# Kernel optimization log

Measured on AMD Instinct MI355X. Metric: run time of the kernel, lower is better.

## Reference

```python
import jax, jax.numpy as jnp
import numpy as np

N = 512          # hidden size n
B = 256          # batch
T = 512          # timesteps
INPUT_SIZE = 2
RANK = 2
ALPHA = 0.2
SIGMA_IN = 0.2
SIGMA_REC = 0.15


def setup_inputs() -> dict:
    key = jax.random.key(0)
    k1, k2, k3, k4, k5, k6 = jax.random.split(key, 6)
    u = jax.random.normal(k1, (B, T, INPUT_SIZE), dtype=jnp.float32)
    # standard normal; scaled by sqrt(2/alpha*sigma_in^2) inside reference
    input_noise = jax.random.normal(k2, (B, T, INPUT_SIZE), dtype=jnp.float32)
    # in the repo this is sigma_rec * randn projected on PCs; plain scaled randn here
    recurrent_noise = SIGMA_REC * jax.random.normal(k3, (B, T, N), dtype=jnp.float32)
    # low-rank recurrent weight: W_rec = A @ B, entries ~ U(-0.1, 0.1)
    A = 0.1 * (2.0 * jax.random.uniform(k4, (N, RANK), dtype=jnp.float32) - 1.0)
    Bm = 0.1 * (2.0 * jax.random.uniform(k5, (RANK, N), dtype=jnp.float32) - 1.0)
    W_rec = A @ Bm
    b_rec = jnp.zeros((N,), dtype=jnp.float32)  # normal_(std=0) -> zeros
    # nn.Linear default init: U(-1/sqrt(in), 1/sqrt(in))
    bound = 1.0 / np.sqrt(INPUT_SIZE)
    W_in = jax.random.uniform(k6, (N, INPUT_SIZE), dtype=jnp.float32,
                              minval=-bound, maxval=bound)
    return {"u": u, "input_noise": input_noise, "recurrent_noise": recurrent_noise,
            "W_in": W_in, "W_rec": W_rec, "b_rec": b_rec}


def reference(u, input_noise, recurrent_noise, W_in, W_rec, b_rec):
    alpha = ALPHA
    in_scale = np.sqrt(2.0 / ALPHA * SIGMA_IN ** 2).astype(np.float32)
    # inputs = input_layer(u + input_noise)  -> [B, T, N]
    inputs = jnp.einsum('bti,ni->btn', u + in_scale * input_noise, W_in)
    # scan over first T-1 timesteps, time-major
    xs = (jnp.swapaxes(inputs, 0, 1)[:-1],          # [T-1, B, N]
          jnp.swapaxes(recurrent_noise, 0, 1)[:-1])  # [T-1, B, N]
    s0 = jnp.zeros((u.shape[0], W_rec.shape[0]), dtype=u.dtype)

    def step(s, x):
        inp_t, noise_t = x
        s_new = (1.0 - alpha) * s + alpha * (
            jax.nn.relu(s) @ W_rec.T + b_rec + inp_t + noise_t)
        return s_new, s_new

    _, ys = jax.lax.scan(step, s0, xs)              # [T-1, B, N]
    states = jnp.concatenate([s0[None], ys], axis=0)  # [T, B, N]
    return jnp.swapaxes(states, 0, 1)               # [B, T, N]
```

## Files before the change

### kernel.cpp

```cpp
#include <hip/hip_runtime.h>
#include <math.h>

#define NH 512
#define BATCH 256
#define TT 512
#define NSTEPS 511
#define ALPHA 0.2f
#define OMA 0.8f
#define ISCALE 0.6324555320336759f
#define PD 12
#define WPB 4

typedef float vf2 __attribute__((ext_vector_type(2)));
typedef float vf4 __attribute__((ext_vector_type(4)));


__device__ __forceinline__ float wave_reduce_sum(float v) {
#pragma unroll
    for (int m = 32; m >= 1; m >>= 1) v += __shfl_xor(v, m, 64);
    return v;
}

__device__ __forceinline__ unsigned long long enc_key(float v, int i) {
    return (((unsigned long long)__float_as_uint(v)) << 32) | (unsigned int)i;
}

__device__ __forceinline__ unsigned long long wave_max_key(unsigned long long k) {
#pragma unroll
    for (int m = 32; m >= 1; m >>= 1) {
        unsigned long long o = __shfl_xor(k, m, 64);
        k = (o > k) ? o : k;
    }
    return k;
}

__device__ __forceinline__ int scan_argmax_rn(const float* __restrict__ rn, int tid) {
    const float4* rn4 = (const float4*)rn;
    unsigned long long key = 0;
#pragma unroll
    for (int r = 0; r < 2; ++r) {
        float4 v = rn4[tid + 64 * r];
        int base = 4 * (tid + 64 * r);
        unsigned long long k0 = enc_key(v.x, base);
        unsigned long long k1 = enc_key(v.y, base + 1);
        unsigned long long k2 = enc_key(v.z, base + 2);
        unsigned long long k3 = enc_key(v.w, base + 3);
        k0 = k0 > k1 ? k0 : k1;
        k2 = k2 > k3 ? k2 : k3;
        k0 = k0 > k2 ? k0 : k2;
        key = key > k0 ? key : k0;
    }
    return (int)(wave_max_key(key) & 0xffffffffULL);
}

__device__ __forceinline__ float dpp_sum63(float v) {
    v += __int_as_float(__builtin_amdgcn_update_dpp(0, __float_as_int(v), 0x111, 0xf, 0xf, true));
    v += __int_as_float(__builtin_amdgcn_update_dpp(0, __float_as_int(v), 0x112, 0xf, 0xf, true));
    v += __int_as_float(__builtin_amdgcn_update_dpp(0, __float_as_int(v), 0x114, 0xf, 0xf, true));
    v += __int_as_float(__builtin_amdgcn_update_dpp(0, __float_as_int(v), 0x118, 0xf, 0xf, true));
    v += __int_as_float(__builtin_amdgcn_update_dpp(0, __float_as_int(v), 0x142, 0xa, 0xf, true));
    v += __int_as_float(__builtin_amdgcn_update_dpp(0, __float_as_int(v), 0x143, 0xc, 0xf, true));
    return v;
}


__global__ void k_rownorm(const float* __restrict__ W, float* __restrict__ rn) {
    const int i = blockIdx.x, tid = threadIdx.x;
    const float4* row = (const float4*)(W + (size_t)i * NH);
    float acc = 0.f;
#pragma unroll
    for (int r = 0; r < 2; ++r) {
        float4 v = row[tid + 64 * r];
        acc = fmaf(v.x, v.x, fmaf(v.y, v.y, fmaf(v.z, v.z, fmaf(v.w, v.w, acc))));
    }
    acc = wave_reduce_sum(acc);
    if (tid == 0) rn[i] = acc;
}

__global__ void k_rowdot(const float* __restrict__ W, const float* __restrict__ rn,
                         float* __restrict__ dv) {
    const int i = blockIdx.x, tid = threadIdx.x;
    const int i1 = scan_argmax_rn(rn, tid);
    const float4* rowi = (const float4*)(W + (size_t)i * NH);
    const float4* row1 = (const float4*)(W + (size_t)i1 * NH);
    float acc = 0.f;
#pragma unroll
    for (int r = 0; r < 2; ++r) {
        float4 a = rowi[tid + 64 * r];
        float4 b = row1[tid + 64 * r];
        acc = fmaf(a.x, b.x, fmaf(a.y, b.y, fmaf(a.z, b.z, fmaf(a.w, b.w, acc))));
    }
    acc = wave_reduce_sum(acc);
    if (tid == 0) dv[i] = acc;
}

__global__ void k_computeP(const float* __restrict__ W, const float* __restrict__ rn,
                           const float* __restrict__ dv, float* __restrict__ P,
                           int* __restrict__ idx) {
    const int n = blockIdx.x, tid = threadIdx.x;
    const int i1 = scan_argmax_rn(rn, tid);
    const float rn1 = rn[i1];
    const float inv1 = 1.f / rn1;

    const float4* rn4 = (const float4*)rn;
    const float4* dv4 = (const float4*)dv;
    unsigned long long key = 0;
#pragma unroll
    for (int r = 0; r < 2; ++r) {
        float4 a = rn4[tid + 64 * r];
        float4 d = dv4[tid + 64 * r];
        int base = 4 * (tid + 64 * r);
        float r0 = fmaxf(a.x - d.x * d.x * inv1, 0.f);
        float r1 = fmaxf(a.y - d.y * d.y * inv1, 0.f);
        float r2 = fmaxf(a.z - d.z * d.z * inv1, 0.f);
        float r3 = fmaxf(a.w - d.w * d.w * inv1, 0.f);
        unsigned long long k0 = (base + 0 != i1) ? enc_key(r0, base + 0) : 0ULL;
        unsigned long long k1 = (base + 1 != i1) ? enc_key(r1, base + 1) : 0ULL;
        unsigned long long k2 = (base + 2 != i1) ? enc_key(r2, base + 2) : 0ULL;
        unsigned long long k3 = (base + 3 != i1) ? enc_key(r3, base + 3) : 0ULL;
        k0 = k0 > k1 ? k0 : k1;
        k2 = k2 > k3 ? k2 : k3;
        k0 = k0 > k2 ? k0 : k2;
        key = key > k0 ? key : k0;
    }
    const int i2 = (int)(wave_max_key(key) & 0xffffffffULL);

    const float4* rown = (const float4*)(W + (size_t)n * NH);
    const float4* row1 = (const float4*)(W + (size_t)i1 * NH);
    const float4* row2 = (const float4*)(W + (size_t)i2 * NH);
    float t0 = 0.f, t1 = 0.f;
#pragma unroll
    for (int r = 0; r < 2; ++r) {
        float4 a = rown[tid + 64 * r];
        float4 b = row1[tid + 64 * r];
        float4 c = row2[tid + 64 * r];
        t0 = fmaf(a.x, b.x, fmaf(a.y, b.y, fmaf(a.z, b.z, fmaf(a.w, b.w, t0))));
        t1 = fmaf(a.x, c.x, fmaf(a.y, c.y, fmaf(a.z, c.z, fmaf(a.w, c.w, t1))));
    }
    t0 = wave_reduce_sum(t0);
    t1 = wave_reduce_sum(t1);
    if (tid == 0) {
        float g11 = rn1, g22 = rn[i2], g12 = dv[i2];
        float det = fmaf(g11, g22, -g12 * g12);
        float inv = 1.f / det;
        P[2 * n]     = ALPHA * ((g22 * t0 - g12 * t1) * inv);
        P[2 * n + 1] = ALPHA * ((g11 * t1 - g12 * t0) * inv);
        if (n == 0) { idx[0] = i1; idx[1] = i2; }
    }
}

__launch_bounds__(256, 1)
__global__ void k_main(const float* __restrict__ u, const float* __restrict__ inoise,
                       const float* __restrict__ rnoise, const float* __restrict__ W_in,
                       const float* __restrict__ W, const float* __restrict__ b_rec,
                       const int* __restrict__ idx, const float* __restrict__ P,
                       float* __restrict__ out) {
    __shared__ __align__(16) float2 lds_x[TT];
    __shared__ __align__(16) float2 lds_p[2][WPB];
    const int b = blockIdx.x;
    const int tid = threadIdx.x;
    const int wid = tid >> 6;
    const int lane = tid & 63;
    const int i1 = idx[0];
    const int i2 = idx[1];

    {
        const float4* u4 = (const float4*)(u + (size_t)b * TT * 2);
        const float4* n4 = (const float4*)(inoise + (size_t)b * TT * 2);
        float4 a = u4[tid];
        float4 c = n4[tid];
        float4 x;
        x.x = fmaf(ISCALE, c.x, a.x);
        x.y = fmaf(ISCALE, c.y, a.y);
        x.z = fmaf(ISCALE, c.z, a.z);
        x.w = fmaf(ISCALE, c.w, a.w);
        ((float4*)lds_x)[tid] = x;
    }
    __syncthreads();

    const int n0 = (wid << 7) + (lane << 1);
    const float q0x = W[(size_t)i1 * NH + n0],     q0y = W[(size_t)i1 * NH + n0 + 1];
    const float q1x = W[(size_t)i2 * NH + n0],     q1y = W[(size_t)i2 * NH + n0 + 1];
    const float A0x = P[2 * n0],                   A1x = P[2 * n0 + 1];
    const float A0y = P[2 * n0 + 2],               A1y = P[2 * n0 + 3];
    const float w0x = ALPHA * W_in[2 * n0],        w1x = ALPHA * W_in[2 * n0 + 1];
    const float w0y = ALPHA * W_in[2 * n0 + 2],    w1y = ALPHA * W_in[2 * n0 + 3];
    const float cbx = ALPHA * b_rec[n0],           cby = ALPHA * b_rec[n0 + 1];
    float sx = 0.f, sy = 0.f;

    const float* nzb = rnoise + (size_t)b * TT * NH + n0;
    float* ob = out + (size_t)b * TT * NH + n0;

    vf2 z = {0.f, 0.f};
    __builtin_nontemporal_store(z, (vf2*)ob);

    vf2 buf[PD];
#pragma unroll
    for (int k = 0; k < PD; ++k) buf[k] = *(const vf2*)(nzb + (size_t)k * NH);

#define STEP(t_, k_, REFILL_, XX_, XY_)                                              \
    {                                                                                \
        const int t = (t_);                                                          \
        vf2 nz = buf[k_];                                                            \
        if (REFILL_) {                                                               \
            int tp = t + PD; if (tp > NSTEPS) tp = NSTEPS;     \
            buf[k_] = *(const vf2*)(nzb + (size_t)tp * NH);                          \
        }                                                                            \
        const float xx = (XX_);                                                      \
        const float xy = (XY_);                                                      \
        float rsx = fmaxf(sx, 0.f), rsy = fmaxf(sy, 0.f);                            \
        float pa = fmaf(rsy, q0y, rsx * q0x);                                        \
        float pb = fmaf(rsy, q1y, rsx * q1x);                                        \
        pa = dpp_sum63(pa);                                                          \
        pb = dpp_sum63(pb);                                                          \
             \
        float bx = fmaf(ALPHA, nz.x, cbx);                                           \
        bx = fmaf(w0x, xx, bx);                                                      \
        bx = fmaf(w1x, xy, bx);                                                      \
        bx = fmaf(OMA, sx, bx);                                                      \
        float by = fmaf(ALPHA, nz.y, cby);                                           \
        by = fmaf(w0y, xx, by);                                                      \
        by = fmaf(w1y, xy, by);                                                      \
        by = fmaf(OMA, sy, by);                                                      \
        if (lane == 63) lds_p[(t) & 1][wid] = make_float2(pa, pb);                   \
        __syncthreads();                                                             \
        const float4* pp = (const float4*)lds_p[(t) & 1];                            \
        float4 r0 = pp[0];                                                           \
        float4 r1 = pp[1];                                                           \
        float p0 = (r0.x + r0.z) + (r1.x + r1.z);                                    \
        float p1 = (r0.y + r0.w) + (r1.y + r1.w);                                    \
        sx = fmaf(A1x, p1, fmaf(A0x, p0, bx));                                       \
        sy = fmaf(A1y, p1, fmaf(A0y, p0, by));                                       \
        vf2 o = {sx, sy};                                                            \
        __builtin_nontemporal_store(o, (vf2*)(ob + (size_t)(t + 1) * NH));           \
    }

    for (int tb = 0; tb < 504; tb += PD) {
        const float4* lxs = (const float4*)(lds_x + tb);
        float4 xb[6];
#pragma unroll
        for (int r = 0; r < 6; ++r) xb[r] = lxs[r];
#pragma unroll
        for (int k = 0; k < PD; ++k) {
            STEP(tb + k, k, true,
                 ((k & 1) ? xb[k >> 1].z : xb[k >> 1].x),
                 ((k & 1) ? xb[k >> 1].w : xb[k >> 1].y))
        }
    }
    {
        const float4* lxs = (const float4*)(lds_x + 504);
        float4 xb[4];
#pragma unroll
        for (int r = 0; r < 4; ++r) xb[r] = lxs[r];
#pragma unroll
        for (int k = 0; k < 7; ++k) {
            STEP(504 + k, k, false,
                 ((k & 1) ? xb[k >> 1].z : xb[k >> 1].x),
                 ((k & 1) ? xb[k >> 1].w : xb[k >> 1].y))
        }
    }

#undef STEP
}


extern "C" void kernel_launch(void* const* d_in, const int* in_sizes, int n_in,
                              void* d_out, int out_size, void* d_ws, size_t ws_size,
                              hipStream_t stream) {
    const float* u      = (const float*)d_in[0];
    const float* inoise = (const float*)d_in[1];
    const float* rnoise = (const float*)d_in[2];
    const float* W_in   = (const float*)d_in[3];
    const float* W      = (const float*)d_in[4];
    const float* b_rec  = (const float*)d_in[5];
    float* out = (float*)d_out;

    char* ws = (char*)d_ws;
    int* idx  = (int*)(ws + 0);
    float* rn = (float*)(ws + 64);
    float* dv = (float*)(ws + 2112);
    float* P  = (float*)(ws + 4160);

    hipLaunchKernelGGL(k_rownorm, dim3(NH), dim3(64), 0, stream, W, rn);
    hipLaunchKernelGGL(k_rowdot, dim3(NH), dim3(64), 0, stream, W, rn, dv);
    hipLaunchKernelGGL(k_computeP, dim3(NH), dim3(64), 0, stream, W, rn, dv, P, idx);
    hipLaunchKernelGGL(k_main, dim3(BATCH), dim3(256), 0, stream,
                       u, inoise, rnoise, W_in, W, b_rec, idx, P, out);
}
```

Before: 470.5 us.

## Fuse setup kernels into one block and use one element per thread

Merges the three projection-setup kernels into a single one-block kernel that keeps row norms and dot products in shared memory, which removes two launches and the workspace round-trips. The main recurrence kernel now uses 512 threads per block, each owning one hidden unit instead of two, and noise is read with nontemporal loads. This spreads per-step work over more waves, at the cost of a wider barrier and a larger cross-wave reduction each step, and the single-block setup serializes work over all rows.

```diff
diff --git a/kernel.cpp b/kernel.cpp
--- a/kernel.cpp
+++ b/kernel.cpp
@@ -9,10 +9,9 @@
 #define OMA 0.8f
 #define ISCALE 0.6324555320336759f
 #define PD 12
-#define WPB 4
+#define WPB 8
 
 typedef float vf2 __attribute__((ext_vector_type(2)));
-typedef float vf4 __attribute__((ext_vector_type(4)));
 
 
 __device__ __forceinline__ float wave_reduce_sum(float v) {
@@ -34,13 +33,13 @@
     return k;
 }
 
-__device__ __forceinline__ int scan_argmax_rn(const float* __restrict__ rn, int tid) {
+__device__ __forceinline__ int scan_argmax_rn(const float* __restrict__ rn, int lane) {
     const float4* rn4 = (const float4*)rn;
     unsigned long long key = 0;
 #pragma unroll
     for (int r = 0; r < 2; ++r) {
-        float4 v = rn4[tid + 64 * r];
-        int base = 4 * (tid + 64 * r);
+        float4 v = rn4[lane + 64 * r];
+        int base = 4 * (lane + 64 * r);
         unsigned long long k0 = enc_key(v.x, base);
         unsigned long long k1 = enc_key(v.y, base + 1);
         unsigned long long k2 = enc_key(v.z, base + 2);
@@ -64,52 +63,54 @@
 }
 
 
-__global__ void k_rownorm(const float* __restrict__ W, float* __restrict__ rn) {
-    const int i = blockIdx.x, tid = threadIdx.x;
-    const float4* row = (const float4*)(W + (size_t)i * NH);
-    float acc = 0.f;
+__global__ __launch_bounds__(256, 1)
+void k_setup(const float* __restrict__ W, float* __restrict__ P, int* __restrict__ idx) {
+    __shared__ __align__(16) float rn_s[NH];
+    __shared__ __align__(16) float dv_s[NH];
+    const int tid = threadIdx.x, wid = tid >> 6, lane = tid & 63;
+
+    for (int row = wid; row < NH; row += 4) {
+        const float4* r4 = (const float4*)(W + (size_t)row * NH);
+        float acc = 0.f;
+#pragma unroll
+        for (int r = 0; r < 2; ++r) {
+            float4 v = r4[lane + 64 * r];
+            acc = fmaf(v.x, v.x, fmaf(v.y, v.y, fmaf(v.z, v.z, fmaf(v.w, v.w, acc))));
+        }
+        acc = wave_reduce_sum(acc);
+        if (lane == 0) rn_s[row] = acc;
+    }
+    __syncthreads();
+
+    const int i1 = scan_argmax_rn(rn_s, lane);
+    const float rn1 = rn_s[i1];
+    const float inv1 = 1.f / rn1;
+
+    const float4* row1 = (const float4*)(W + (size_t)i1 * NH);
+    const float4 b0 = row1[lane], b1 = row1[lane + 64];
+
+    for (int row = wid; row < NH; row += 4) {
+        const float4* r4 = (const float4*)(W + (size_t)row * NH);
+        float acc = 0.f;
+        {
+            float4 a = r4[lane];
+            acc = fmaf(a.x, b0.x, fmaf(a.y, b0.y, fmaf(a.z, b0.z, fmaf(a.w, b0.w, acc))));
+            a = r4[lane + 64];
+            acc = fmaf(a.x, b1.x, fmaf(a.y, b1.y, fmaf(a.z, b1.z, fmaf(a.w, b1.w, acc))));
+        }
+        acc = wave_reduce_sum(acc);
+        if (lane == 0) dv_s[row] = acc;
+    }
+    __syncthreads();
+
+    const float4* rn4 = (const float4*)rn_s;
+    const float4* dv4 = (const float4*)dv_s;
+    unsigned long long key = 0;
 #pragma unroll
     for (int r = 0; r < 2; ++r) {
-        float4 v = row[tid + 64 * r];
-        acc = fmaf(v.x, v.x, fmaf(v.y, v.y, fmaf(v.z, v.z, fmaf(v.w, v.w, acc))));
-    }
-    acc = wave_reduce_sum(acc);
-    if (tid == 0) rn[i] = acc;
-}
-
-__global__ void k_rowdot(const float* __restrict__ W, const float* __restrict__ rn,
-                         float* __restrict__ dv) {
-    const int i = blockIdx.x, tid = threadIdx.x;
-    const int i1 = scan_argmax_rn(rn, tid);
-    const float4* rowi = (const float4*)(W + (size_t)i * NH);
-    const float4* row1 = (const float4*)(W + (size_t)i1 * NH);
-    float acc = 0.f;
-#pragma unroll
-    for (int r = 0; r < 2; ++r) {
-        float4 a = rowi[tid + 64 * r];
-        float4 b = row1[tid + 64 * r];
-        acc = fmaf(a.x, b.x, fmaf(a.y, b.y, fmaf(a.z, b.z, fmaf(a.w, b.w, acc))));
-    }
-    acc = wave_reduce_sum(acc);
-    if (tid == 0) dv[i] = acc;
-}
-
-__global__ void k_computeP(const float* __restrict__ W, const float* __restrict__ rn,
-                           const float* __restrict__ dv, float* __restrict__ P,
-                           int* __restrict__ idx) {
-    const int n = blockIdx.x, tid = threadIdx.x;
-    const int i1 = scan_argmax_rn(rn, tid);
-    const float rn1 = rn[i1];
-    const float inv1 = 1.f / rn1;
-
-    const float4* rn4 = (const float4*)rn;
-    const float4* dv4 = (const float4*)dv;
-    unsigned long long key = 0;
-#pragma unroll
-    for (int r = 0; r < 2; ++r) {
-        float4 a = rn4[tid + 64 * r];
-        float4 d = dv4[tid + 64 * r];
-        int base = 4 * (tid + 64 * r);
+        float4 a = rn4[lane + 64 * r];
+        float4 d = dv4[lane + 64 * r];
+        int base = 4 * (lane + 64 * r);
         float r0 = fmaxf(a.x - d.x * d.x * inv1, 0.f);
         float r1 = fmaxf(a.y - d.y * d.y * inv1, 0.f);
         float r2 = fmaxf(a.z - d.z * d.z * inv1, 0.f);
@@ -125,31 +126,33 @@
     }
     const int i2 = (int)(wave_max_key(key) & 0xffffffffULL);
 
-    const float4* rown = (const float4*)(W + (size_t)n * NH);
-    const float4* row1 = (const float4*)(W + (size_t)i1 * NH);
     const float4* row2 = (const float4*)(W + (size_t)i2 * NH);
-    float t0 = 0.f, t1 = 0.f;
-#pragma unroll
-    for (int r = 0; r < 2; ++r) {
-        float4 a = rown[tid + 64 * r];
-        float4 b = row1[tid + 64 * r];
-        float4 c = row2[tid + 64 * r];
-        t0 = fmaf(a.x, b.x, fmaf(a.y, b.y, fmaf(a.z, b.z, fmaf(a.w, b.w, t0))));
-        t1 = fmaf(a.x, c.x, fmaf(a.y, c.y, fmaf(a.z, c.z, fmaf(a.w, c.w, t1))));
-    }
-    t0 = wave_reduce_sum(t0);
-    t1 = wave_reduce_sum(t1);
-    if (tid == 0) {
-        float g11 = rn1, g22 = rn[i2], g12 = dv[i2];
-        float det = fmaf(g11, g22, -g12 * g12);
-        float inv = 1.f / det;
-        P[2 * n]     = ALPHA * ((g22 * t0 - g12 * t1) * inv);
-        P[2 * n + 1] = ALPHA * ((g11 * t1 - g12 * t0) * inv);
-        if (n == 0) { idx[0] = i1; idx[1] = i2; }
-    }
-}
-
-__launch_bounds__(256, 1)
+    const float4 c0 = row2[lane], c1 = row2[lane + 64];
+    const float g11 = rn1, g22 = rn_s[i2], g12 = dv_s[i2];
+    const float det = fmaf(g11, g22, -g12 * g12);
+    const float invd = 1.f / det;
+    for (int row = wid; row < NH; row += 4) {
+        const float4* r4 = (const float4*)(W + (size_t)row * NH);
+        float t0 = 0.f, t1 = 0.f;
+        {
+            float4 a = r4[lane];
+            t0 = fmaf(a.x, b0.x, fmaf(a.y, b0.y, fmaf(a.z, b0.z, fmaf(a.w, b0.w, t0))));
+            t1 = fmaf(a.x, c0.x, fmaf(a.y, c0.y, fmaf(a.z, c0.z, fmaf(a.w, c0.w, t1))));
+            a = r4[lane + 64];
+            t0 = fmaf(a.x, b1.x, fmaf(a.y, b1.y, fmaf(a.z, b1.z, fmaf(a.w, b1.w, t0))));
+            t1 = fmaf(a.x, c1.x, fmaf(a.y, c1.y, fmaf(a.z, c1.z, fmaf(a.w, c1.w, t1))));
+        }
+        t0 = wave_reduce_sum(t0);
+        t1 = wave_reduce_sum(t1);
+        if (lane == 0) {
+            P[2 * row]     = ALPHA * ((g22 * t0 - g12 * t1) * invd);
+            P[2 * row + 1] = ALPHA * ((g11 * t1 - g12 * t0) * invd);
+        }
+    }
+    if (tid == 0) { idx[0] = i1; idx[1] = i2; }
+}
+
+__launch_bounds__(512, 1)
 __global__ void k_main(const float* __restrict__ u, const float* __restrict__ inoise,
                        const float* __restrict__ rnoise, const float* __restrict__ W_in,
                        const float* __restrict__ W, const float* __restrict__ b_rec,
@@ -165,74 +168,67 @@
     const int i2 = idx[1];
 
     {
-        const float4* u4 = (const float4*)(u + (size_t)b * TT * 2);
-        const float4* n4 = (const float4*)(inoise + (size_t)b * TT * 2);
-        float4 a = u4[tid];
-        float4 c = n4[tid];
-        float4 x;
+        const float2* u2 = (const float2*)(u + (size_t)b * TT * 2);
+        const float2* n2 = (const float2*)(inoise + (size_t)b * TT * 2);
+        float2 a = u2[tid];
+        float2 c = n2[tid];
+        float2 x;
         x.x = fmaf(ISCALE, c.x, a.x);
         x.y = fmaf(ISCALE, c.y, a.y);
-        x.z = fmaf(ISCALE, c.z, a.z);
-        x.w = fmaf(ISCALE, c.w, a.w);
-        ((float4*)lds_x)[tid] = x;
+        lds_x[tid] = x;
     }
     __syncthreads();
 
-    const int n0 = (wid << 7) + (lane << 1);
-    const float q0x = W[(size_t)i1 * NH + n0],     q0y = W[(size_t)i1 * NH + n0 + 1];
-    const float q1x = W[(size_t)i2 * NH + n0],     q1y = W[(size_t)i2 * NH + n0 + 1];
-    const float A0x = P[2 * n0],                   A1x = P[2 * n0 + 1];
-    const float A0y = P[2 * n0 + 2],               A1y = P[2 * n0 + 3];
-    const float w0x = ALPHA * W_in[2 * n0],        w1x = ALPHA * W_in[2 * n0 + 1];
-    const float w0y = ALPHA * W_in[2 * n0 + 2],    w1y = ALPHA * W_in[2 * n0 + 3];
-    const float cbx = ALPHA * b_rec[n0],           cby = ALPHA * b_rec[n0 + 1];
-    float sx = 0.f, sy = 0.f;
+    const int n0 = (wid << 6) + lane;
+    const float q0 = W[(size_t)i1 * NH + n0];
+    const float q1 = W[(size_t)i2 * NH + n0];
+    const float A0 = P[2 * n0];
+    const float A1 = P[2 * n0 + 1];
+    const float w0 = ALPHA * W_in[2 * n0];
+    const float w1 = ALPHA * W_in[2 * n0 + 1];
+    const float cb = ALPHA * b_rec[n0];
+    float s = 0.f;
 
     const float* nzb = rnoise + (size_t)b * TT * NH + n0;
     float* ob = out + (size_t)b * TT * NH + n0;
 
-    vf2 z = {0.f, 0.f};
-    __builtin_nontemporal_store(z, (vf2*)ob);
-
-    vf2 buf[PD];
-#pragma unroll
-    for (int k = 0; k < PD; ++k) buf[k] = *(const vf2*)(nzb + (size_t)k * NH);
+    __builtin_nontemporal_store(0.f, ob);
+
+    float buf[PD];
+#pragma unroll
+    for (int k = 0; k < PD; ++k) buf[k] = __builtin_nontemporal_load(nzb + (size_t)k * NH);
 
 #define STEP(t_, k_, REFILL_, XX_, XY_)                                              \
     {                                                                                \
         const int t = (t_);                                                          \
-        vf2 nz = buf[k_];                                                            \
+        float nz = buf[k_];                                                          \
         if (REFILL_) {                                                               \
             int tp = t + PD; if (tp > NSTEPS) tp = NSTEPS;     \
-            buf[k_] = *(const vf2*)(nzb + (size_t)tp * NH);                          \
+            buf[k_] = __builtin_nontemporal_load(nzb + (size_t)tp * NH);             \
         }                                                                            \
         const float xx = (XX_);                                                      \
         const float xy = (XY_);                                                      \
-        float rsx = fmaxf(sx, 0.f), rsy = fmaxf(sy, 0.f);                            \
-        float pa = fmaf(rsy, q0y, rsx * q0x);                                        \
-        float pb = fmaf(rsy, q1y, rsx * q1x);                                        \
+        float rs = fmaxf(s, 0.f);                                                    \
+        float pa = rs * q0;                                                          \
+        float pb = rs * q1;                                                          \
         pa = dpp_sum63(pa);                                                          \
         pb = dpp_sum63(pb);                                                          \
              \
-        float bx = fmaf(ALPHA, nz.x, cbx);                                           \
-        bx = fmaf(w0x, xx, bx);                                                      \
-        bx = fmaf(w1x, xy, bx);                                                      \
-        bx = fmaf(OMA, sx, bx);                                                      \
-        float by = fmaf(ALPHA, nz.y, cby);                                           \
-        by = fmaf(w0y, xx, by);                                                      \
-        by = fmaf(w1y, xy, by);                                                      \
-        by = fmaf(OMA, sy, by);                                                      \
+        float base = fmaf(ALPHA, nz, cb);                                            \
+        base = fmaf(w0, xx, base);                                                   \
+        base = fmaf(w1, xy, base);                                                   \
+        base = fmaf(OMA, s, base);                                                   \
         if (lane == 63) lds_p[(t) & 1][wid] = make_float2(pa, pb);                   \
         __syncthreads();                                                             \
         const float4* pp = (const float4*)lds_p[(t) & 1];                            \
         float4 r0 = pp[0];                                                           \
         float4 r1 = pp[1];                                                           \
-        float p0 = (r0.x + r0.z) + (r1.x + r1.z);                                    \
-        float p1 = (r0.y + r0.w) + (r1.y + r1.w);                                    \
-        sx = fmaf(A1x, p1, fmaf(A0x, p0, bx));                                       \
-        sy = fmaf(A1y, p1, fmaf(A0y, p0, by));                                       \
-        vf2 o = {sx, sy};                                                            \
-        __builtin_nontemporal_store(o, (vf2*)(ob + (size_t)(t + 1) * NH));           \
+        float4 r2 = pp[2];                                                           \
+        float4 r3 = pp[3];                                                           \
+        float p0 = ((r0.x + r0.z) + (r1.x + r1.z)) + ((r2.x + r2.z) + (r3.x + r3.z));\
+        float p1 = ((r0.y + r0.w) + (r1.y + r1.w)) + ((r2.y + r2.w) + (r3.y + r3.w));\
+        s = fmaf(A1, p1, fmaf(A0, p0, base));                                        \
+        __builtin_nontemporal_store(s, ob + (size_t)(t + 1) * NH);                   \
     }
 
     for (int tb = 0; tb < 504; tb += PD) {
@@ -277,13 +273,9 @@
 
     char* ws = (char*)d_ws;
     int* idx  = (int*)(ws + 0);
-    float* rn = (float*)(ws + 64);
-    float* dv = (float*)(ws + 2112);
-    float* P  = (float*)(ws + 4160);
-
-    hipLaunchKernelGGL(k_rownorm, dim3(NH), dim3(64), 0, stream, W, rn);
-    hipLaunchKernelGGL(k_rowdot, dim3(NH), dim3(64), 0, stream, W, rn, dv);
-    hipLaunchKernelGGL(k_computeP, dim3(NH), dim3(64), 0, stream, W, rn, dv, P, idx);
-    hipLaunchKernelGGL(k_main, dim3(BATCH), dim3(256), 0, stream,
+    float* P  = (float*)(ws + 64);
+
+    hipLaunchKernelGGL(k_setup, dim3(1), dim3(256), 0, stream, W, P, idx);
+    hipLaunchKernelGGL(k_main, dim3(BATCH), dim3(512), 0, stream,
                        u, inoise, rnoise, W_in, W, b_rec, idx, P, out);
 }
```

Result: slower. 707.5 us (+50.4%).

## Use one hidden unit per thread with 512-thread blocks and lighter barrier

Applied to the files above, without the earlier changes.

Doubles the block to 512 threads so each thread owns a single hidden unit instead of two. This shortens the per-step dependent arithmetic and spreads the global loads and stores over more waves. The cross-wave partial sums now cover eight waves, and __syncthreads is replaced by an explicit lgkmcnt wait plus s_barrier. The cost is a barrier across eight waves instead of four, scalar rather than vector memory accesses, and a slightly longer LDS reduction at every step.

```diff
diff --git a/kernel.cpp b/kernel.cpp
--- a/kernel.cpp
+++ b/kernel.cpp
@@ -9,10 +9,9 @@
 #define OMA 0.8f
 #define ISCALE 0.6324555320336759f
 #define PD 12
-#define WPB 4
+#define WPB 8
 
 typedef float vf2 __attribute__((ext_vector_type(2)));
-typedef float vf4 __attribute__((ext_vector_type(4)));
 
 
 __device__ __forceinline__ float wave_reduce_sum(float v) {
@@ -149,7 +148,7 @@
     }
 }
 
-__launch_bounds__(256, 1)
+__launch_bounds__(512, 1)
 __global__ void k_main(const float* __restrict__ u, const float* __restrict__ inoise,
                        const float* __restrict__ rnoise, const float* __restrict__ W_in,
                        const float* __restrict__ W, const float* __restrict__ b_rec,
@@ -165,74 +164,70 @@
     const int i2 = idx[1];
 
     {
-        const float4* u4 = (const float4*)(u + (size_t)b * TT * 2);
-        const float4* n4 = (const float4*)(inoise + (size_t)b * TT * 2);
-        float4 a = u4[tid];
-        float4 c = n4[tid];
-        float4 x;
+        const float2* u2 = (const float2*)(u + (size_t)b * TT * 2);
+        const float2* n2 = (const float2*)(inoise + (size_t)b * TT * 2);
+        float2 a = u2[tid];
+        float2 c = n2[tid];
+        float2 x;
         x.x = fmaf(ISCALE, c.x, a.x);
         x.y = fmaf(ISCALE, c.y, a.y);
-        x.z = fmaf(ISCALE, c.z, a.z);
-        x.w = fmaf(ISCALE, c.w, a.w);
-        ((float4*)lds_x)[tid] = x;
+        lds_x[tid] = x;
     }
     __syncthreads();
 
-    const int n0 = (wid << 7) + (lane << 1);
-    const float q0x = W[(size_t)i1 * NH + n0],     q0y = W[(size_t)i1 * NH + n0 + 1];
-    const float q1x = W[(size_t)i2 * NH + n0],     q1y = W[(size_t)i2 * NH + n0 + 1];
-    const float A0x = P[2 * n0],                   A1x = P[2 * n0 + 1];
-    const float A0y = P[2 * n0 + 2],               A1y = P[2 * n0 + 3];
-    const float w0x = ALPHA * W_in[2 * n0],        w1x = ALPHA * W_in[2 * n0 + 1];
-    const float w0y = ALPHA * W_in[2 * n0 + 2],    w1y = ALPHA * W_in[2 * n0 + 3];
-    const float cbx = ALPHA * b_rec[n0],           cby = ALPHA * b_rec[n0 + 1];
-    float sx = 0.f, sy = 0.f;
+    const int n0 = (wid << 6) + lane;
+    const float q0 = W[(size_t)i1 * NH + n0];
+    const float q1 = W[(size_t)i2 * NH + n0];
+    const float A0 = P[2 * n0];
+    const float A1 = P[2 * n0 + 1];
+    const float w0 = ALPHA * W_in[2 * n0];
+    const float w1 = ALPHA * W_in[2 * n0 + 1];
+    const float cb = ALPHA * b_rec[n0];
+    float s = 0.f;
 
     const float* nzb = rnoise + (size_t)b * TT * NH + n0;
     float* ob = out + (size_t)b * TT * NH + n0;
 
-    vf2 z = {0.f, 0.f};
-    __builtin_nontemporal_store(z, (vf2*)ob);
-
-    vf2 buf[PD];
-#pragma unroll
-    for (int k = 0; k < PD; ++k) buf[k] = *(const vf2*)(nzb + (size_t)k * NH);
+    __builtin_nontemporal_store(0.f, ob);
+
+    float buf[PD];
+#pragma unroll
+    for (int k = 0; k < PD; ++k) buf[k] = nzb[(size_t)k * NH];
 
 #define STEP(t_, k_, REFILL_, XX_, XY_)                                              \
     {                                                                                \
         const int t = (t_);                                                          \
-        vf2 nz = buf[k_];                                                            \
+        float nz = buf[k_];                                                          \
         if (REFILL_) {                                                               \
             int tp = t + PD; if (tp > NSTEPS) tp = NSTEPS;     \
-            buf[k_] = *(const vf2*)(nzb + (size_t)tp * NH);                          \
+            buf[k_] = nzb[(size_t)tp * NH];                                          \
         }                                                                            \
         const float xx = (XX_);                                                      \
         const float xy = (XY_);                                                      \
-        float rsx = fmaxf(sx, 0.f), rsy = fmaxf(sy, 0.f);                            \
-        float pa = fmaf(rsy, q0y, rsx * q0x);                                        \
-        float pb = fmaf(rsy, q1y, rsx * q1x);                                        \
+        float rs = fmaxf(s, 0.f);                                                    \
+        float pa = rs * q0;                                                          \
+        float pb = rs * q1;                                                          \
         pa = dpp_sum63(pa);                                                          \
         pb = dpp_sum63(pb);                                                          \
              \
-        float bx = fmaf(ALPHA, nz.x, cbx);                                           \
-        bx = fmaf(w0x, xx, bx);                                                      \
-        bx = fmaf(w1x, xy, bx);                                                      \
-        bx = fmaf(OMA, sx, bx);                                                      \
-        float by = fmaf(ALPHA, nz.y, cby);                                           \
-        by = fmaf(w0y, xx, by);                                                      \
-        by = fmaf(w1y, xy, by);                                                      \
-        by = fmaf(OMA, sy, by);                                                      \
+        float base = fmaf(ALPHA, nz, cb);                                            \
+        base = fmaf(w0, xx, base);                                                   \
+        base = fmaf(w1, xy, base);                                                   \
+        base = fmaf(OMA, s, base);                                                   \
         if (lane == 63) lds_p[(t) & 1][wid] = make_float2(pa, pb);                   \
-        __syncthreads();                                                             \
+           \
+        asm volatile("s_waitcnt lgkmcnt(0)" ::: "memory");                           \
+        __builtin_amdgcn_s_barrier();                                                \
+        asm volatile("" ::: "memory");                                               \
         const float4* pp = (const float4*)lds_p[(t) & 1];                            \
         float4 r0 = pp[0];                                                           \
         float4 r1 = pp[1];                                                           \
-        float p0 = (r0.x + r0.z) + (r1.x + r1.z);                                    \
-        float p1 = (r0.y + r0.w) + (r1.y + r1.w);                                    \
-        sx = fmaf(A1x, p1, fmaf(A0x, p0, bx));                                       \
-        sy = fmaf(A1y, p1, fmaf(A0y, p0, by));                                       \
-        vf2 o = {sx, sy};                                                            \
-        __builtin_nontemporal_store(o, (vf2*)(ob + (size_t)(t + 1) * NH));           \
+        float4 r2 = pp[2];                                                           \
+        float4 r3 = pp[3];                                                           \
+        float p0 = ((r0.x + r0.z) + (r1.x + r1.z)) + ((r2.x + r2.z) + (r3.x + r3.z));\
+        float p1 = ((r0.y + r0.w) + (r1.y + r1.w)) + ((r2.y + r2.w) + (r3.y + r3.w));\
+        s = fmaf(A1, p1, fmaf(A0, p0, base));                                        \
+        __builtin_nontemporal_store(s, ob + (size_t)(t + 1) * NH);                   \
     }
 
     for (int tb = 0; tb < 504; tb += PD) {
@@ -284,6 +279,6 @@
     hipLaunchKernelGGL(k_rownorm, dim3(NH), dim3(64), 0, stream, W, rn);
     hipLaunchKernelGGL(k_rowdot, dim3(NH), dim3(64), 0, stream, W, rn, dv);
     hipLaunchKernelGGL(k_computeP, dim3(NH), dim3(64), 0, stream, W, rn, dv, P, idx);
-    hipLaunchKernelGGL(k_main, dim3(BATCH), dim3(256), 0, stream,
+    hipLaunchKernelGGL(k_main, dim3(BATCH), dim3(512), 0, stream,
                        u, inoise, rnoise, W_in, W, b_rec, idx, P, out);
 }
```

Result: slower. 523.0 us (+11.1%).
